# Performance work log

Hardware: AMD Instinct MI355X
Metric: run time of the kernel (lower is better)

The kernel has to match this reference:

```python
import jax, jax.numpy as jnp
import numpy as np

# SamplesLoss('sinkhorn', p=2, blur=0.05, scaling=0.5, diameter=2.0, debias=True, backend='tensorized')
P = 2
BLUR = 0.05
SCALING = 0.5
DIAMETER = 2.0


def epsilon_schedule(p, diameter, blur, scaling):
    # geomloss epsilon annealing: diameter^p -> blur^p, geometric in eps
    eps_list = (
        [diameter ** p]
        + [np.exp(e) for e in np.arange(p * np.log(diameter), p * np.log(blur), p * np.log(scaling))]
        + [blur ** p]
    )
    return [float(e) for e in eps_list]


def softmin(eps, C, h):
    # soft C-transform: f_i = -eps * log sum_j exp(h_j - C_ij/eps)
    # C: (B,N,M), h: (B,M) -> (B,N)
    return -eps * jax.scipy.special.logsumexp(h[:, None, :] - C / eps, axis=2)


def sq_cost(x, y):
    # SqDist(x,y)/2 : (B,N,D),(B,M,D) -> (B,N,M)
    x2 = jnp.sum(x * x, axis=-1)[:, :, None]
    y2 = jnp.sum(y * y, axis=-1)[:, None, :]
    return (x2 + y2 - 2.0 * jnp.einsum('bnd,bmd->bnm', x, y)) * 0.5


def setup_inputs() -> dict:
    key = jax.random.key(0)
    k1, k2 = jax.random.split(key)
    x = jax.random.uniform(k1, (8, 2048, 3), dtype=jnp.float32)
    y = jax.random.uniform(k2, (8, 2048, 3), dtype=jnp.float32)
    return {"x": x, "y": y}


def reference(x, y):
    B, N, _ = x.shape
    M = y.shape[1]
    # uniform weights (SamplesLoss default when only point clouds are given)
    a_log = jnp.full((B, N), -float(np.log(N)), dtype=x.dtype)
    b_log = jnp.full((B, M), -float(np.log(M)), dtype=y.dtype)

    C_xy = sq_cost(x, y)                 # (B,N,M)
    C_yx = jnp.swapaxes(C_xy, 1, 2)      # (B,M,N)
    C_xx = sq_cost(x, x)                 # (B,N,N) debias term
    C_yy = sq_cost(y, y)                 # (B,M,M) debias term

    eps_list = epsilon_schedule(P, DIAMETER, BLUR, SCALING)

    # initialization at the coarsest temperature (balanced OT: damping = 1)
    eps0 = eps_list[0]
    f_aa = softmin(eps0, C_xx, a_log)
    g_bb = softmin(eps0, C_yy, b_log)
    g_ab = softmin(eps0, C_yx, a_log)
    f_ba = softmin(eps0, C_xy, b_log)

    # symmetric Sinkhorn loop with epsilon scaling (no grad tracked in torch here)
    for eps in eps_list:
        ft_ba = softmin(eps, C_xy, b_log + g_ab / eps)
        gt_ab = softmin(eps, C_yx, a_log + f_ba / eps)
        f_ba = 0.5 * (f_ba + ft_ba)
        g_ab = 0.5 * (g_ab + gt_ab)
        ft_aa = softmin(eps, C_xx, a_log + f_aa / eps)
        gt_bb = softmin(eps, C_yy, b_log + g_bb / eps)
        f_aa = 0.5 * (f_aa + ft_aa)
        g_bb = 0.5 * (g_bb + gt_bb)

    # last extrapolation step, with detached dual potentials (torch .detach())
    eps = eps_list[-1]
    sg = jax.lax.stop_gradient
    f_ba, g_ab = (
        softmin(eps, C_xy, b_log + sg(g_ab) / eps),
        softmin(eps, C_yx, a_log + sg(f_ba) / eps),
    )
    f_aa = softmin(eps, C_xx, a_log + sg(f_aa) / eps)
    g_bb = softmin(eps, C_yy, b_log + sg(g_bb) / eps)

    # debiased Sinkhorn divergence, batch mode -> (B,)
    a = jnp.exp(a_log)
    b = jnp.exp(b_log)
    return jnp.sum(a * (f_ba - f_aa), axis=-1) + jnp.sum(b * (g_ab - g_bb), axis=-1)
```

## Files before the change

### kernel.cpp

```cpp
#include <hip/hip_runtime.h>
#include <math.h>

#define BATCH 8
#define NPTS 2048
#define THREADS 256
#define HALF_COLS 1024
#define TILES_H 32
#define ROWS_PER_BLOCK 64
#define LOG_M 7.62559580411076

typedef __attribute__((ext_vector_type(8)))  __bf16 bf16x8;
typedef __attribute__((ext_vector_type(16))) float  f32x16;
typedef __attribute__((ext_vector_type(2)))  float  f32x2;

union FragU { unsigned short u[8]; uint4 v; };

__device__ __forceinline__ unsigned short f2bf(float f) {
    union { float f; unsigned u; } x; x.f = f;
    unsigned r = x.u + 0x7FFFu + ((x.u >> 16) & 1u);
    return (unsigned short)(r >> 16);
}
__device__ __forceinline__ float bf2f(unsigned short b) {
    union { unsigned u; float f; } x; x.u = ((unsigned)b) << 16;
    return x.f;
}

__global__ __launch_bounds__(THREADS) void softmin_pass(
    const float* __restrict__ x, const float* __restrict__ y,
    const float* __restrict__ potSrc, float* __restrict__ potDst,
    uint4* __restrict__ CF0, uint2* __restrict__ CF1, float* __restrict__ YSQ,
    float sigma, float k2, float inv_k2, float rowc0,
    int avg, int first, int last, float* __restrict__ out)
{
    __shared__ uint4 BF[TILES_H][64];
    __shared__ uint4 AF[2][64];
    __shared__ float NM[ROWS_PER_BLOCK];

    const int type  = blockIdx.z;
    const int batch = blockIdx.y;

    const float* rowP;
    const float* colP;
    int hslot, oslot, cs;
    if (type == 0)      { rowP = x; colP = y; hslot = 1; oslot = 0; cs = 1; }
    else if (type == 1) { rowP = y; colP = x; hslot = 0; oslot = 1; cs = 0; }
    else if (type == 2) { rowP = x; colP = x; hslot = 2; oslot = 2; cs = 0; }
    else                { rowP = y; colP = y; hslot = 3; oslot = 3; cs = 1; }

    rowP += batch * NPTS * 3;
    colP += batch * NPTS * 3;
    const float* hP   = potSrc + (hslot * BATCH + batch) * NPTS;
    const float* oldP = potSrc + (oslot * BATCH + batch) * NPTS;
    float*       outP = potDst + (oslot * BATCH + batch) * NPTS;
    const size_t cbase = ((size_t)cs * BATCH + batch) * NPTS;

    if (threadIdx.x < 128) {
        const int g = threadIdx.x >> 6, idx = threadIdx.x & 63;
        const int row = blockIdx.x * ROWS_PER_BLOCK + g * 32 + (idx & 31);
        float x0 = rowP[3 * row + 0], x1 = rowP[3 * row + 1], x2 = rowP[3 * row + 2];
        float p0 = sigma * (x0 - 0.5f), p1 = sigma * (x1 - 0.5f), p2 = sigma * (x2 - 0.5f);
        unsigned short h0 = f2bf(p0); unsigned short l0 = f2bf(p0 - bf2f(h0));
        unsigned short h1 = f2bf(p1); unsigned short l1 = f2bf(p1 - bf2f(h1));
        unsigned short h2 = f2bf(p2); unsigned short l2 = f2bf(p2 - bf2f(h2));
        FragU f;
        if (idx < 32) {
            f.u[0] = h0; f.u[1] = h0; f.u[2] = l0; f.u[3] = l0;
            f.u[4] = h1; f.u[5] = h1; f.u[6] = l1; f.u[7] = l1;
        } else {
            f.u[0] = h2; f.u[1] = h2; f.u[2] = l2; f.u[3] = l2;
            f.u[4] = 0x3F80; f.u[5] = 0x3F80; f.u[6] = 0x3F80; f.u[7] = 0;
        }
        AF[g][idx] = f.v;
    } else if (threadIdx.x < 128 + ROWS_PER_BLOCK) {
        const int r = threadIdx.x - 128;
        const int i = blockIdx.x * ROWS_PER_BLOCK + r;
        float x0 = rowP[3 * i + 0], x1 = rowP[3 * i + 1], x2 = rowP[3 * i + 2];
        float p0 = x0 - 0.5f, p1 = x1 - 0.5f, p2 = x2 - 0.5f;
        float rowconst = 0.5f * (p0 * p0 + p1 * p1 + p2 * p2) + rowc0;
        float oldv = first ? 0.0f : oldP[i];
        NM[r] = (oldv - rowconst) * inv_k2;
    }

    const int lane = threadIdx.x & 63;
    const int wave = threadIdx.x >> 6;
    const int g    = wave >> 1;
    const int c    = wave & 1;
    const int khalf = lane >> 5;

    f32x2 sp[8];
    #pragma unroll
    for (int q = 0; q < 8; ++q) { sp[q].x = 0.0f; sp[q].y = 0.0f; }
    bf16x8 af;
    f32x16 nmv;

    for (int h = 0; h < 2; ++h) {
        if (h) __syncthreads();

        if (first) {
            const int writer = (blockIdx.x == 0) && (type <= 1);
            for (int jj = threadIdx.x; jj < HALF_COLS; jj += THREADS) {
                const int j = h * HALF_COLS + jj;
                float y0 = colP[3 * j + 0], y1 = colP[3 * j + 1], y2 = colP[3 * j + 2];
                float p0 = y0 - 0.5f, p1 = y1 - 0.5f, p2 = y2 - 0.5f;
                unsigned short h0 = f2bf(p0); unsigned short l0 = f2bf(p0 - bf2f(h0));
                unsigned short h1 = f2bf(p1); unsigned short l1 = f2bf(p1 - bf2f(h1));
                unsigned short h2 = f2bf(p2); unsigned short l2 = f2bf(p2 - bf2f(h2));
                float ysq = 0.5f * (p0 * p0 + p1 * p1 + p2 * p2);
                float hhe = -sigma * ysq;
                unsigned short hA = f2bf(hhe); float r1 = hhe - bf2f(hA);
                unsigned short hB = f2bf(r1);  float r2 = r1 - bf2f(hB);
                unsigned short hC = f2bf(r2);
                FragU f0, f1;
                f0.u[0] = h0; f0.u[1] = l0; f0.u[2] = h0; f0.u[3] = l0;
                f0.u[4] = h1; f0.u[5] = l1; f0.u[6] = h1; f0.u[7] = l1;
                f1.u[0] = h2; f1.u[1] = l2; f1.u[2] = h2; f1.u[3] = l2;
                f1.u[4] = hA; f1.u[5] = hB; f1.u[6] = hC; f1.u[7] = 0;
                BF[jj >> 5][jj & 31]        = f0.v;
                BF[jj >> 5][32 + (jj & 31)] = f1.v;
                if (writer) {
                    CF0[cbase + j] = f0.v;
                    CF1[cbase + j] = make_uint2(f1.v.x, f1.v.y);
                    YSQ[cbase + j] = ysq;
                }
            }
        } else {
            for (int jj = threadIdx.x; jj < HALF_COLS; jj += THREADS) {
                const int j = h * HALF_COLS + jj;
                uint4 f0  = CF0[cbase + j];
                uint2 f1l = CF1[cbase + j];
                float hhe = sigma * (hP[j] - YSQ[cbase + j]);
                unsigned short hA = f2bf(hhe); float r1 = hhe - bf2f(hA);
                unsigned short hB = f2bf(r1);  float r2 = r1 - bf2f(hB);
                unsigned short hC = f2bf(r2);
                uint4 f1 = make_uint4(f1l.x, f1l.y,
                                      (unsigned)hA | ((unsigned)hB << 16),
                                      (unsigned)hC);
                BF[jj >> 5][jj & 31]        = f0;
                BF[jj >> 5][32 + (jj & 31)] = f1;
            }
        }
        __syncthreads();

        if (h == 0) {
            af = *(const bf16x8*)&AF[g][lane];
            #pragma unroll
            for (int r = 0; r < 16; ++r) {
                const int row = (r & 3) + 8 * (r >> 2) + 4 * khalf;
                nmv[r] = NM[g * 32 + row];
            }
        }

        const int tbase = c * (TILES_H / 2);
        #pragma unroll 2
        for (int t = 0; t < TILES_H / 2; ++t) {
            bf16x8 bf = *(const bf16x8*)&BF[tbase + t][lane];
            f32x16 acc = __builtin_amdgcn_mfma_f32_32x32x16_bf16(af, bf, nmv, 0, 0, 0);
            #pragma unroll
            for (int q = 0; q < 8; ++q) {
                f32x2 e;
                e.x = __builtin_amdgcn_exp2f(acc[2 * q]);
                e.y = __builtin_amdgcn_exp2f(acc[2 * q + 1]);
                asm("v_pk_add_f32 %0, %0, %1" : "+v"(sp[q]) : "v"(e));
            }
        }
    }

    __syncthreads();
    {
        f32x2* SP = (f32x2*)&BF[0][0];
        #pragma unroll
        for (int q = 0; q < 8; ++q)
            SP[(q * 4 + wave) * 64 + (lane ^ ((q & 3) << 3))] = sp[q];
    }
    __syncthreads();

    {
        const float* SPf = (const float*)&BF[0][0];
        const int v  = threadIdx.x >> 2;
        const int p  = threadIdx.x & 3;
        const int gg = v >> 5, vv = v & 31;
        const int kh = (vv >> 2) & 1;
        const int r  = (vv & 3) | ((vv >> 3) << 2);
        const int q  = r >> 1, comp = r & 1;
        const int sw = (q & 3) << 3;
        float val = 0.0f;
        #pragma unroll
        for (int cc = 0; cc < 2; ++cc) {
            const int w = gg * 2 + cc;
            #pragma unroll
            for (int jj = 0; jj < 8; ++jj) {
                const int j = p * 8 + ((jj + v) & 7);
                const int l = kh * 32 + j;
                val += SPf[(((q * 4 + w) * 64) + (l ^ sw)) * 2 + comp];
            }
        }
        val += __shfl_xor(val, 1, 64);
        val += __shfl_xor(val, 2, 64);
        if (p == 0) {
            const int i = blockIdx.x * ROWS_PER_BLOCK + v;
            float oldv = first ? 0.0f : oldP[i];
            float res  = oldv - k2 * __log2f(val);
            outP[i] = avg ? 0.5f * (oldv + res) : res;
            if (last) NM[v] = res;
        }
    }

    if (last) {
        __syncthreads();
        if (wave == 0) {
            float v2 = NM[lane];
            #pragma unroll
            for (int off = 32; off >= 1; off >>= 1)
                v2 += __shfl_xor(v2, off, 64);
            if (lane == 0) {
                float sign = (type >= 2) ? -1.0f : 1.0f;
                atomicAdd(out + batch, sign * v2 * (1.0f / NPTS));
            }
        }
    }
}

extern "C" void kernel_launch(void* const* d_in, const int* in_sizes, int n_in,
                              void* d_out, int out_size, void* d_ws, size_t ws_size,
                              hipStream_t stream)
{
    const float* x = (const float*)d_in[0];
    const float* y = (const float*)d_in[1];
    float* out = (float*)d_out;

    const size_t potElems = (size_t)4 * BATCH * NPTS;
    const size_t colElems = (size_t)2 * BATCH * NPTS;
    float* P0  = (float*)d_ws;
    float* P1  = P0 + potElems;
    uint4* CF0 = (uint4*)(P1 + potElems);
    uint2* CF1 = (uint2*)(CF0 + colElems);
    float* YSQ = (float*)(CF1 + colElems);

    hipMemsetAsync(out, 0, BATCH * sizeof(float), stream);

    double epsl[16];
    int ne = 0;
    epsl[ne++] = 4.0;
    const double stop = 2.0 * log(0.05);
    const double step = 2.0 * log(0.5);
    for (double e = 2.0 * log(2.0); e > stop; e += step)
        epsl[ne++] = exp(e);
    epsl[ne++] = 0.05 * 0.05;

    float* src = P0;
    float* dst = P1;
    dim3 grid(NPTS / ROWS_PER_BLOCK, BATCH, 4);

    auto launch = [&](double eps, int avg, int first, int last) {
        float sigma  = (float)(M_LOG2E / eps);
        float k2     = (float)(eps * M_LN2);
        float inv_k2 = (float)(1.0 / (eps * M_LN2));
        float rowc0  = (float)(eps * LOG_M);
        softmin_pass<<<grid, THREADS, 0, stream>>>(
            x, y, src, dst, CF0, CF1, YSQ,
            sigma, k2, inv_k2, rowc0, avg, first, last, out);
        float* t = src; src = dst; dst = t;
    };

    launch(epsl[0], 0, 1, 0);
    for (int k = 0; k < ne; ++k)
        launch(epsl[k], 1, 0, 0);
    launch(epsl[ne - 1], 0, 0, 1);
}
```

Measured before the change: 256.0 us.

## Double rows per block so each wave covers all column tiles; pack ysq into CF1

Each block now handles 128 rows, and each of its four waves owns 32 rows and loops over all 32 column tiles. Before, two waves split the column tiles for the same row group. This halves the grid and halves how often each column tile is staged into shared memory per row, cutting the per-block column preparation and the reduction work. The separate YSQ array is dropped: ysq is stored in the second word of CF1, and the duplicated h2/l2 word is rebuilt from the first word. The risk is fewer blocks (512 instead of 1024) and a longer serial MFMA+exp loop per wave, which could reduce latency hiding.

```diff
diff --git a/kernel.cpp b/kernel.cpp
--- a/kernel.cpp
+++ b/kernel.cpp
@@ -6,7 +6,7 @@
 #define THREADS 256
 #define HALF_COLS 1024
 #define TILES_H 32
-#define ROWS_PER_BLOCK 64
+#define ROWS_PER_BLOCK 128
 #define LOG_M 7.62559580411076
 
 typedef __attribute__((ext_vector_type(8)))  __bf16 bf16x8;
@@ -25,15 +25,15 @@
     return x.f;
 }
 
-__global__ __launch_bounds__(THREADS) void softmin_pass(
+__global__ __launch_bounds__(THREADS, 2) void softmin_pass(
     const float* __restrict__ x, const float* __restrict__ y,
     const float* __restrict__ potSrc, float* __restrict__ potDst,
-    uint4* __restrict__ CF0, uint2* __restrict__ CF1, float* __restrict__ YSQ,
+    uint4* __restrict__ CF0, uint2* __restrict__ CF1,
     float sigma, float k2, float inv_k2, float rowc0,
     int avg, int first, int last, float* __restrict__ out)
 {
     __shared__ uint4 BF[TILES_H][64];
-    __shared__ uint4 AF[2][64];
+    __shared__ uint4 AF[4][64];
     __shared__ float NM[ROWS_PER_BLOCK];
 
     const int type  = blockIdx.z;
@@ -54,9 +54,9 @@
     float*       outP = potDst + (oslot * BATCH + batch) * NPTS;
     const size_t cbase = ((size_t)cs * BATCH + batch) * NPTS;
 
-    if (threadIdx.x < 128) {
-        const int g = threadIdx.x >> 6, idx = threadIdx.x & 63;
-        const int row = blockIdx.x * ROWS_PER_BLOCK + g * 32 + (idx & 31);
+    {
+        const int gg = threadIdx.x >> 6, idx = threadIdx.x & 63;
+        const int row = blockIdx.x * ROWS_PER_BLOCK + gg * 32 + (idx & 31);
         float x0 = rowP[3 * row + 0], x1 = rowP[3 * row + 1], x2 = rowP[3 * row + 2];
         float p0 = sigma * (x0 - 0.5f), p1 = sigma * (x1 - 0.5f), p2 = sigma * (x2 - 0.5f);
         unsigned short h0 = f2bf(p0); unsigned short l0 = f2bf(p0 - bf2f(h0));
@@ -70,9 +70,10 @@
             f.u[0] = h2; f.u[1] = h2; f.u[2] = l2; f.u[3] = l2;
             f.u[4] = 0x3F80; f.u[5] = 0x3F80; f.u[6] = 0x3F80; f.u[7] = 0;
         }
-        AF[g][idx] = f.v;
-    } else if (threadIdx.x < 128 + ROWS_PER_BLOCK) {
-        const int r = threadIdx.x - 128;
+        AF[gg][idx] = f.v;
+    }
+    if (threadIdx.x < ROWS_PER_BLOCK) {
+        const int r = threadIdx.x;
         const int i = blockIdx.x * ROWS_PER_BLOCK + r;
         float x0 = rowP[3 * i + 0], x1 = rowP[3 * i + 1], x2 = rowP[3 * i + 2];
         float p0 = x0 - 0.5f, p1 = x1 - 0.5f, p2 = x2 - 0.5f;
@@ -82,9 +83,7 @@
     }
 
     const int lane = threadIdx.x & 63;
-    const int wave = threadIdx.x >> 6;
-    const int g    = wave >> 1;
-    const int c    = wave & 1;
+    const int g    = threadIdx.x >> 6;
     const int khalf = lane >> 5;
 
     f32x2 sp[8];
@@ -119,8 +118,7 @@
                 BF[jj >> 5][32 + (jj & 31)] = f1.v;
                 if (writer) {
                     CF0[cbase + j] = f0.v;
-                    CF1[cbase + j] = make_uint2(f1.v.x, f1.v.y);
-                    YSQ[cbase + j] = ysq;
+                    CF1[cbase + j] = make_uint2(f1.v.x, __float_as_uint(ysq));
                 }
             }
         } else {
@@ -128,11 +126,12 @@
                 const int j = h * HALF_COLS + jj;
                 uint4 f0  = CF0[cbase + j];
                 uint2 f1l = CF1[cbase + j];
-                float hhe = sigma * (hP[j] - YSQ[cbase + j]);
+                float ysq = __uint_as_float(f1l.y);
+                float hhe = sigma * (hP[j] - ysq);
                 unsigned short hA = f2bf(hhe); float r1 = hhe - bf2f(hA);
                 unsigned short hB = f2bf(r1);  float r2 = r1 - bf2f(hB);
                 unsigned short hC = f2bf(r2);
-                uint4 f1 = make_uint4(f1l.x, f1l.y,
+                uint4 f1 = make_uint4(f1l.x, f1l.x,
                                       (unsigned)hA | ((unsigned)hB << 16),
                                       (unsigned)hC);
                 BF[jj >> 5][jj & 31]        = f0;
@@ -150,10 +149,9 @@
             }
         }
 
-        const int tbase = c * (TILES_H / 2);
         #pragma unroll 2
-        for (int t = 0; t < TILES_H / 2; ++t) {
-            bf16x8 bf = *(const bf16x8*)&BF[tbase + t][lane];
+        for (int t = 0; t < TILES_H; ++t) {
+            bf16x8 bf = *(const bf16x8*)&BF[t][lane];
             f32x16 acc = __builtin_amdgcn_mfma_f32_32x32x16_bf16(af, bf, nmv, 0, 0, 0);
             #pragma unroll
             for (int q = 0; q < 8; ++q) {
@@ -170,14 +168,14 @@
         f32x2* SP = (f32x2*)&BF[0][0];
         #pragma unroll
         for (int q = 0; q < 8; ++q)
-            SP[(q * 4 + wave) * 64 + (lane ^ ((q & 3) << 3))] = sp[q];
+            SP[(q * 4 + g) * 64 + (lane ^ ((q & 3) << 3))] = sp[q];
     }
     __syncthreads();
 
     {
         const float* SPf = (const float*)&BF[0][0];
-        const int v  = threadIdx.x >> 2;
-        const int p  = threadIdx.x & 3;
+        const int v  = threadIdx.x >> 1;
+        const int p  = threadIdx.x & 1;
         const int gg = v >> 5, vv = v & 31;
         const int kh = (vv >> 2) & 1;
         const int r  = (vv & 3) | ((vv >> 3) << 2);
@@ -185,17 +183,12 @@
         const int sw = (q & 3) << 3;
         float val = 0.0f;
         #pragma unroll
-        for (int cc = 0; cc < 2; ++cc) {
-            const int w = gg * 2 + cc;
-            #pragma unroll
-            for (int jj = 0; jj < 8; ++jj) {
-                const int j = p * 8 + ((jj + v) & 7);
-                const int l = kh * 32 + j;
-                val += SPf[(((q * 4 + w) * 64) + (l ^ sw)) * 2 + comp];
-            }
+        for (int jj = 0; jj < 16; ++jj) {
+            const int j = (p * 16 + jj + v) & 31;
+            const int l = kh * 32 + j;
+            val += SPf[(((q * 4 + gg) * 64) + (l ^ sw)) * 2 + comp];
         }
         val += __shfl_xor(val, 1, 64);
-        val += __shfl_xor(val, 2, 64);
         if (p == 0) {
             const int i = blockIdx.x * ROWS_PER_BLOCK + v;
             float oldv = first ? 0.0f : oldP[i];
@@ -207,8 +200,8 @@
 
     if (last) {
         __syncthreads();
-        if (wave == 0) {
-            float v2 = NM[lane];
+        if (g == 0) {
+            float v2 = NM[lane] + NM[64 + lane];
             #pragma unroll
             for (int off = 32; off >= 1; off >>= 1)
                 v2 += __shfl_xor(v2, off, 64);
@@ -234,7 +227,6 @@
     float* P1  = P0 + potElems;
     uint4* CF0 = (uint4*)(P1 + potElems);
     uint2* CF1 = (uint2*)(CF0 + colElems);
-    float* YSQ = (float*)(CF1 + colElems);
 
     hipMemsetAsync(out, 0, BATCH * sizeof(float), stream);
 
@@ -257,7 +249,7 @@
         float inv_k2 = (float)(1.0 / (eps * M_LN2));
         float rowc0  = (float)(eps * LOG_M);
         softmin_pass<<<grid, THREADS, 0, stream>>>(
-            x, y, src, dst, CF0, CF1, YSQ,
+            x, y, src, dst, CF0, CF1,
             sigma, k2, inv_k2, rowc0, avg, first, last, out);
         float* t = src; src = dst; dst = t;
     };
```

Measured after the change: 232.5 us, median of 2. 1.1x faster.
